# Performance work log

Measured on AMD Instinct MI355X. Metric: run time of the kernel, lower is better.

The kernel has to match this reference:

```python
import jax, jax.numpy as jnp
import numpy as np

DIM = 1024
NUM_HEADS = 16
HEAD_DIM = DIM // NUM_HEADS


def setup_inputs() -> dict:
    key = jax.random.key(0)
    ks = jax.random.split(key, 16)
    B, Sx, Sy = 4, 1024, 1024
    s = 1.0 / np.sqrt(DIM)
    inp = {
        'x': jax.random.normal(ks[0], (B, Sx, DIM), dtype=jnp.float32),
        'y': jax.random.normal(ks[1], (B, Sy, DIM), dtype=jnp.float32),
    }
    names = ['Kx', 'Qx', 'Vx', 'Ky', 'Vy', 'out']
    for i, n in enumerate(names):
        inp[f'W_{n}'] = jax.random.uniform(ks[2 + 2 * i], (DIM, DIM), dtype=jnp.float32, minval=-s, maxval=s)
        inp[f'b_{n}'] = jax.random.uniform(ks[3 + 2 * i], (DIM,), dtype=jnp.float32, minval=-s, maxval=s)
    return inp


def _heads(t, B, S):
    # [B, S, DIM] -> [B, H, S, Dh]
    return t.reshape(B, S, NUM_HEADS, HEAD_DIM).transpose(0, 2, 1, 3)


def _attn(x, y, W_Kx, b_Kx, W_Qx, b_Qx, W_Vx, b_Vx, W_Ky, b_Ky, W_Vy, b_Vy, W_out, b_out):
    B, Sx, _ = x.shape
    Sy = y.shape[1]
    lin = lambda t, W, b: t @ W.T + b
    Q = _heads(lin(x, W_Qx, b_Qx), B, Sx)
    Kc = jnp.concatenate([_heads(lin(x, W_Kx, b_Kx), B, Sx), _heads(lin(y, W_Ky, b_Ky), B, Sy)], axis=2)
    Vc = jnp.concatenate([_heads(lin(x, W_Vx, b_Vx), B, Sx), _heads(lin(y, W_Vy, b_Vy), B, Sy)], axis=2)
    scores = jnp.einsum('bhqd,bhkd->bhqk', Q, Kc) / np.sqrt(HEAD_DIM).astype(np.float32)
    w = jax.nn.softmax(scores, axis=-1)
    o = jnp.einsum('bhqk,bhkd->bhqd', w, Vc)  # [B, H, Sx, Dh]
    o = o.transpose(0, 2, 1, 3).reshape(B, Sx, DIM)
    return lin(o, W_out, b_out)


def reference(x, y, W_Kx, b_Kx, W_Qx, b_Qx, W_Vx, b_Vx, W_Ky, b_Ky, W_Vy, b_Vy, W_out, b_out):
    return _attn(x, y, W_Kx, b_Kx, W_Qx, b_Qx, W_Vx, b_Vx, W_Ky, b_Ky, W_Vy, b_Vy, W_out, b_out)
```

## Files before the change

### kernel.cpp

```cpp
#include <hip/hip_runtime.h>

#define DIMN 1024
#define NH 16
#define DH 64
#define SXX 1024
#define SKV 2048

typedef __bf16 bf16x8 __attribute__((ext_vector_type(8)));
typedef float f32x4 __attribute__((ext_vector_type(4)));
typedef unsigned short us8 __attribute__((ext_vector_type(8)));

__device__ __forceinline__ unsigned short f2bs(float f) {
    return (unsigned short)((__builtin_bit_cast(unsigned int, f) + 0x8000u) >> 16);
}
__device__ __forceinline__ void gl_lds16(const void* g, void* l) {
    __builtin_amdgcn_global_load_lds(
        (const __attribute__((address_space(1))) unsigned int*)g,
        (__attribute__((address_space(3))) unsigned int*)l, 16, 0, 0);
}

struct CvtArgs {
    const float* src[8];
    unsigned short* dst[8];
    int start[8];
};
__global__ __launch_bounds__(256) void cvt_all(CvtArgs a) {
    int b = blockIdx.x;
    int r = 0;
#pragma unroll
    for (int i = 1; i < 8; i++) r += (b >= a.start[i]);
    int off = ((b - a.start[r]) * 256 + (int)threadIdx.x) * 8;
    const float* s = a.src[r] + off;
    float4 f0 = *(const float4*)(s);
    float4 f1 = *(const float4*)(s + 4);
    us8 o;
    o[0] = f2bs(f0.x); o[1] = f2bs(f0.y); o[2] = f2bs(f0.z); o[3] = f2bs(f0.w);
    o[4] = f2bs(f1.x); o[5] = f2bs(f1.y); o[6] = f2bs(f1.z); o[7] = f2bs(f1.w);
    *(us8*)(a.dst[r] + off) = o;
}

template<int KIND>
__global__ void gemm_fused(const unsigned short* __restrict__ A,
                           const unsigned short* __restrict__ W,
                           const float* __restrict__ b0, const float* __restrict__ b1,
                           const float* __restrict__ b2,
                           unsigned short* __restrict__ Qd, unsigned short* __restrict__ Kd,
                           unsigned short* __restrict__ Vd, int roff, float qscale,
                           float* __restrict__ outp) {
    __shared__ __align__(16) unsigned short As[128 * 32];
    __shared__ __align__(16) unsigned short Bs[128 * 32];
    const int K = DIMN;
    int tid = threadIdx.x, wave = tid >> 6, lane = tid & 63;
    int l15 = lane & 15, quad = lane >> 4;
    int wm = wave >> 1, wn = wave & 1;
    int m0 = blockIdx.y * 128, n0 = blockIdx.x * 128;

    int srow = wave * 16 + (lane >> 2);
    int sc8 = (lane & 3) * 8;
    const unsigned short* gA0 = A + (size_t)(m0 + srow) * K + sc8;
    const unsigned short* gA1 = A + (size_t)(m0 + srow + 64) * K + sc8;
    const unsigned short* gW0 = W + (size_t)(n0 + srow) * K + sc8;
    const unsigned short* gW1 = W + (size_t)(n0 + srow + 64) * K + sc8;
    unsigned short* lA0 = As + wave * 512;
    unsigned short* lA1 = As + 2048 + wave * 512;
    unsigned short* lB0 = Bs + wave * 512;
    unsigned short* lB1 = Bs + 2048 + wave * 512;

    f32x4 acc[4][4] = {};
    for (int k0 = 0; k0 < K; k0 += 32) {
        if (k0) __syncthreads();
        gl_lds16(gA0 + k0, lA0);
        gl_lds16(gA1 + k0, lA1);
        gl_lds16(gW0 + k0, lB0);
        gl_lds16(gW1 + k0, lB1);
        __syncthreads();
        bf16x8 af[4], bf[4];
#pragma unroll
        for (int mi = 0; mi < 4; mi++)
            af[mi] = __builtin_bit_cast(bf16x8, *(const us8*)(&As[(wm * 64 + mi * 16 + l15) * 32 + quad * 8]));
#pragma unroll
        for (int ni = 0; ni < 4; ni++)
            bf[ni] = __builtin_bit_cast(bf16x8, *(const us8*)(&Bs[(wn * 64 + ni * 16 + l15) * 32 + quad * 8]));
#pragma unroll
        for (int mi = 0; mi < 4; mi++)
#pragma unroll
            for (int ni = 0; ni < 4; ni++)
                acc[mi][ni] = __builtin_amdgcn_mfma_f32_16x16x32_bf16(af[mi], bf[ni], acc[mi][ni], 0, 0, 0);
    }

    int which = n0 >> 10;
    const float* bp = (which == 0) ? b0 : (which == 1) ? b1 : b2;
    int role;
    if (KIND == 2) role = 3;
    else if (KIND == 1) role = which ? 2 : 0;
    else role = (which == 0) ? 0 : (which == 1) ? 1 : 2;
    float sc = (role == 1) ? qscale : 1.0f;

#pragma unroll
    for (int mi = 0; mi < 4; mi++) {
        int mbase = m0 + wm * 64 + mi * 16 + quad * 4;
#pragma unroll
        for (int ni = 0; ni < 4; ni++) {
            int n = n0 + wn * 64 + ni * 16 + l15;
            int nl = n & 1023;
            float bv = bp[nl];
#pragma unroll
            for (int r = 0; r < 4; r++) {
                float v = (acc[mi][ni][r] + bv) * sc;
                int mm = mbase + r;
                int bidx = mm >> 10, s = mm & 1023, h = nl >> 6, d = nl & 63;
                if (role == 3) {
                    outp[(size_t)mm * DIMN + n] = v;
                } else if (role == 0) {
                    Kd[((size_t)(bidx * NH + h) * SKV + s + roff) * DH + d] = f2bs(v);
                } else if (role == 1) {
                    Qd[((size_t)(bidx * NH + h) * SXX + s) * DH + d] = f2bs(v);
                } else {
                    Vd[((size_t)(bidx * NH + h) * DH + d) * SKV + s + roff] = f2bs(v);
                }
            }
        }
    }
}

__global__ __launch_bounds__(256, 4) void flash_attn(
        const unsigned short* __restrict__ Qb,
        const unsigned short* __restrict__ Kc,
        const unsigned short* __restrict__ Vt,
        unsigned short* __restrict__ Ob) {
    __shared__ __align__(16) unsigned short Ks[2][64 * 64];
    __shared__ __align__(16) unsigned short Vs[2][64 * 64];
    __shared__ __align__(16) unsigned short Ps[4][16 * 64];
    int tid = threadIdx.x, wave = tid >> 6, lane = tid & 63;
    int l15 = lane & 15, quad = lane >> 4;
    int bh = blockIdx.y;
    int qbase = blockIdx.x * 64 + wave * 16;

    const unsigned short* Qp = Qb + ((size_t)bh * SXX + qbase) * DH;
    bf16x8 bq0 = __builtin_bit_cast(bf16x8, *(const us8*)(&Qp[l15 * DH + quad * 8]));
    bf16x8 bq1 = __builtin_bit_cast(bf16x8, *(const us8*)(&Qp[l15 * DH + 32 + quad * 8]));

    const unsigned short* Kg = Kc + (size_t)bh * SKV * DH;
    const unsigned short* Vg = Vt + (size_t)bh * DH * SKV;

    int srow_lo = 8 * wave + (lane >> 3);
    int srow_hi = srow_lo + 32;
    int swz = ((lane & 7) ^ (lane >> 3)) * 8;
    int sl = (lane & 7) * 8;

    us8 pk0, pk1, pv0, pv1;
    auto gload = [&](int c) {
        pk0 = *(const us8*)(Kg + (size_t)(c + srow_lo) * DH + swz);
        pk1 = *(const us8*)(Kg + (size_t)(c + srow_hi) * DH + swz);
        pv0 = *(const us8*)(Vg + (size_t)srow_lo * SKV + c + swz);
        pv1 = *(const us8*)(Vg + (size_t)srow_hi * SKV + c + swz);
    };
    auto lstore = [&](int buf) {
        *(us8*)(&Ks[buf][srow_lo * 64 + sl]) = pk0;
        *(us8*)(&Ks[buf][srow_hi * 64 + sl]) = pk1;
        *(us8*)(&Vs[buf][srow_lo * 64 + sl]) = pv0;
        *(us8*)(&Vs[buf][srow_hi * 64 + sl]) = pv1;
    };

    f32x4 o[4] = {};
    float lsum = 0.0f;

    gload(0);
    lstore(0);
    __syncthreads();

    for (int c = 0; c < SKV; c += 64) {
        int cur = (c >> 6) & 1;
        bool more = (c + 64) < SKV;
        if (more) gload(c + 64);

        const unsigned short* ks = &Ks[cur][0];
        f32x4 st[4];
        int cA = quad ^ (l15 & 7);
#pragma unroll
        for (int ni = 0; ni < 4; ni++) {
            int row = (ni * 16 + l15) * 64;
            bf16x8 ak0 = __builtin_bit_cast(bf16x8, *(const us8*)(ks + row + cA * 8));
            bf16x8 ak1 = __builtin_bit_cast(bf16x8, *(const us8*)(ks + row + (cA ^ 4) * 8));
            f32x4 z = {};
            z = __builtin_amdgcn_mfma_f32_16x16x32_bf16(ak0, bq0, z, 0, 0, 0);
            z = __builtin_amdgcn_mfma_f32_16x16x32_bf16(ak1, bq1, z, 0, 0, 0);
            st[ni] = z;
        }

        unsigned short* pw = &Ps[wave][0];
#pragma unroll
        for (int ni = 0; ni < 4; ni++) {
            float p0 = __builtin_amdgcn_exp2f(st[ni][0]);
            float p1 = __builtin_amdgcn_exp2f(st[ni][1]);
            float p2 = __builtin_amdgcn_exp2f(st[ni][2]);
            float p3 = __builtin_amdgcn_exp2f(st[ni][3]);
            lsum += (p0 + p1) + (p2 + p3);
            unsigned int lo = ((__builtin_bit_cast(unsigned int, p0) + 0x8000u) >> 16)
                            | ((__builtin_bit_cast(unsigned int, p1) + 0x8000u) & 0xffff0000u);
            unsigned int hi = ((__builtin_bit_cast(unsigned int, p2) + 0x8000u) >> 16)
                            | ((__builtin_bit_cast(unsigned int, p3) + 0x8000u) & 0xffff0000u);
            int c8p = (2 * ni + (quad >> 1)) ^ (l15 & 7);
            *(uint2*)(pw + l15 * 64 + c8p * 8 + (quad & 1) * 4) = make_uint2(lo, hi);
        }

        bf16x8 ap0 = __builtin_bit_cast(bf16x8, *(const us8*)(pw + l15 * 64 + cA * 8));
        bf16x8 ap1 = __builtin_bit_cast(bf16x8, *(const us8*)(pw + l15 * 64 + (cA ^ 4) * 8));

        const unsigned short* vs = &Vs[cur][0];
#pragma unroll
        for (int ni = 0; ni < 4; ni++) {
            int row = (ni * 16 + l15) * 64;
            bf16x8 v0 = __builtin_bit_cast(bf16x8, *(const us8*)(vs + row + cA * 8));
            bf16x8 v1 = __builtin_bit_cast(bf16x8, *(const us8*)(vs + row + (cA ^ 4) * 8));
            o[ni] = __builtin_amdgcn_mfma_f32_16x16x32_bf16(ap0, v0, o[ni], 0, 0, 0);
            o[ni] = __builtin_amdgcn_mfma_f32_16x16x32_bf16(ap1, v1, o[ni], 0, 0, 0);
        }

        if (more) lstore(1 - cur);
        __syncthreads();
    }

    lsum += __shfl_xor(lsum, 16);
    lsum += __shfl_xor(lsum, 32);
    int b = bh >> 4, h = bh & 15;
#pragma unroll
    for (int r = 0; r < 4; r++) {
        float lt = __shfl(lsum, quad * 4 + r);
        float inv = __builtin_amdgcn_rcpf(lt);
        int q = qbase + quad * 4 + r;
#pragma unroll
        for (int ni = 0; ni < 4; ni++)
            Ob[((size_t)b * SXX + q) * DIMN + h * DH + ni * 16 + l15] = f2bs(o[ni][r] * inv);
    }
}

extern "C" void kernel_launch(void* const* d_in, const int* in_sizes, int n_in,
                              void* d_out, int out_size, void* d_ws, size_t ws_size,
                              hipStream_t stream) {
    (void)in_sizes; (void)n_in; (void)out_size; (void)ws_size;
    const float* x     = (const float*)d_in[0];
    const float* y     = (const float*)d_in[1];
    const float* W_Kx  = (const float*)d_in[2];
    const float* b_Kx  = (const float*)d_in[3];
    const float* W_Qx  = (const float*)d_in[4];
    const float* b_Qx  = (const float*)d_in[5];
    const float* W_Vx  = (const float*)d_in[6];
    const float* b_Vx  = (const float*)d_in[7];
    const float* W_Ky  = (const float*)d_in[8];
    const float* b_Ky  = (const float*)d_in[9];
    const float* W_Vy  = (const float*)d_in[10];
    const float* b_Vy  = (const float*)d_in[11];
    const float* W_out = (const float*)d_in[12];
    const float* b_out = (const float*)d_in[13];
    float* out = (float*)d_out;

    char* ws = (char*)d_ws;
    unsigned short* xb  = (unsigned short*)(ws);
    unsigned short* yb  = (unsigned short*)(ws + (size_t)( 8 << 20));
    unsigned short* Qb  = (unsigned short*)(ws + (size_t)(16 << 20));
    unsigned short* Kcw = (unsigned short*)(ws + (size_t)(24 << 20));
    unsigned short* Vtw = (unsigned short*)(ws + (size_t)(40 << 20));
    unsigned short* Obw = (unsigned short*)(ws + (size_t)(56 << 20));
    unsigned short* Wb  = (unsigned short*)(ws + (size_t)(64 << 20));

    CvtArgs ca;
    ca.src[0] = x;     ca.dst[0] = xb;                 ca.start[0] = 0;
    ca.src[1] = y;     ca.dst[1] = yb;                 ca.start[1] = 2048;
    ca.src[2] = W_Kx;  ca.dst[2] = Wb + 0u * 1048576;  ca.start[2] = 4096;
    ca.src[3] = W_Qx;  ca.dst[3] = Wb + 1u * 1048576;  ca.start[3] = 4608;
    ca.src[4] = W_Vx;  ca.dst[4] = Wb + 2u * 1048576;  ca.start[4] = 5120;
    ca.src[5] = W_Ky;  ca.dst[5] = Wb + 3u * 1048576;  ca.start[5] = 5632;
    ca.src[6] = W_Vy;  ca.dst[6] = Wb + 4u * 1048576;  ca.start[6] = 6144;
    ca.src[7] = W_out; ca.dst[7] = Wb + 5u * 1048576;  ca.start[7] = 6656;
    cvt_all<<<7168, 256, 0, stream>>>(ca);

    const float qscale = 0.125f * 1.44269504088896340736f;
    gemm_fused<0><<<dim3(24, 32), 256, 0, stream>>>(xb, Wb, b_Kx, b_Qx, b_Vx,
                                                    Qb, Kcw, Vtw, 0, qscale, nullptr);
    gemm_fused<1><<<dim3(16, 32), 256, 0, stream>>>(yb, Wb + 3u * 1048576, b_Ky, b_Vy, nullptr,
                                                    Qb, Kcw, Vtw, 1024, 1.0f, nullptr);
    flash_attn<<<dim3(16, 64), 256, 0, stream>>>(Qb, Kcw, Vtw, Obw);
    gemm_fused<2><<<dim3(8, 32), 256, 0, stream>>>(Obw, Wb + 5u * 1048576, b_out, nullptr, nullptr,
                                                   nullptr, nullptr, nullptr, 0, 1.0f, out);
}
```

Measured before the change: 276.5 us.

## Restructure projection GEMMs and double query tile per wave in attention

```diff
diff --git a/kernel.cpp b/kernel.cpp
--- a/kernel.cpp
+++ b/kernel.cpp
@@ -39,106 +39,176 @@
     *(us8*)(a.dst[r] + off) = o;
 }
 
-template<int KIND>
-__global__ void gemm_fused(const unsigned short* __restrict__ A,
-                           const unsigned short* __restrict__ W,
-                           const float* __restrict__ b0, const float* __restrict__ b1,
-                           const float* __restrict__ b2,
-                           unsigned short* __restrict__ Qd, unsigned short* __restrict__ Kd,
-                           unsigned short* __restrict__ Vd, int roff, float qscale,
-                           float* __restrict__ outp) {
-    __shared__ __align__(16) unsigned short As[128 * 32];
-    __shared__ __align__(16) unsigned short Bs[128 * 32];
+__device__ __forceinline__ void gemm_core(const unsigned short* __restrict__ A,
+                                          const unsigned short* __restrict__ W,
+                                          unsigned short* As, unsigned short* Bs,
+                                          int m0, int n0, f32x4 (&acc)[4][4]) {
     const int K = DIMN;
     int tid = threadIdx.x, wave = tid >> 6, lane = tid & 63;
     int l15 = lane & 15, quad = lane >> 4;
     int wm = wave >> 1, wn = wave & 1;
-    int m0 = blockIdx.y * 128, n0 = blockIdx.x * 128;
-
-    int srow = wave * 16 + (lane >> 2);
-    int sc8 = (lane & 3) * 8;
-    const unsigned short* gA0 = A + (size_t)(m0 + srow) * K + sc8;
-    const unsigned short* gA1 = A + (size_t)(m0 + srow + 64) * K + sc8;
-    const unsigned short* gW0 = W + (size_t)(n0 + srow) * K + sc8;
-    const unsigned short* gW1 = W + (size_t)(n0 + srow + 64) * K + sc8;
-    unsigned short* lA0 = As + wave * 512;
-    unsigned short* lA1 = As + 2048 + wave * 512;
-    unsigned short* lB0 = Bs + wave * 512;
-    unsigned short* lB1 = Bs + 2048 + wave * 512;
+    int srow = wave * 8 + (lane >> 3);
+    int gcol = ((lane & 7) ^ (lane >> 3)) * 8;
+    const unsigned short* gA = A + (size_t)(m0 + srow) * K + gcol;
+    const unsigned short* gW = W + (size_t)(n0 + srow) * K + gcol;
+    unsigned short* lA = As + wave * 512;
+    unsigned short* lB = Bs + wave * 512;
+    int slot0 = (quad ^ (l15 & 7)) * 8;
+
+    for (int k0 = 0; k0 < K; k0 += 64) {
+        if (k0) __syncthreads();
+#pragma unroll
+        for (int j = 0; j < 4; j++) {
+            gl_lds16(gA + k0 + (size_t)j * 32 * K, lA + j * 2048);
+            gl_lds16(gW + k0 + (size_t)j * 32 * K, lB + j * 2048);
+        }
+        __syncthreads();
+#pragma unroll
+        for (int kk = 0; kk < 2; kk++) {
+            int sl = slot0 ^ (kk * 32);
+            bf16x8 af[4], bf[4];
+#pragma unroll
+            for (int mi = 0; mi < 4; mi++)
+                af[mi] = __builtin_bit_cast(bf16x8, *(const us8*)(&As[(wm * 64 + mi * 16 + l15) * 64 + sl]));
+#pragma unroll
+            for (int ni = 0; ni < 4; ni++)
+                bf[ni] = __builtin_bit_cast(bf16x8, *(const us8*)(&Bs[(wn * 64 + ni * 16 + l15) * 64 + sl]));
+#pragma unroll
+            for (int mi = 0; mi < 4; mi++)
+#pragma unroll
+                for (int ni = 0; ni < 4; ni++)
+                    acc[mi][ni] = __builtin_amdgcn_mfma_f32_16x16x32_bf16(af[mi], bf[ni], acc[mi][ni], 0, 0, 0);
+        }
+    }
+}
+
+__global__ __launch_bounds__(256, 2) void gemm_kq(
+        const unsigned short* __restrict__ xb, const unsigned short* __restrict__ yb,
+        const unsigned short* __restrict__ Wb,
+        const float* __restrict__ b_Kx, const float* __restrict__ b_Qx, const float* __restrict__ b_Ky,
+        unsigned short* __restrict__ Qd, unsigned short* __restrict__ Kd, float qscale) {
+    __shared__ __align__(16) unsigned short As[128 * 64];
+    __shared__ __align__(16) unsigned short Bs[128 * 64];
+    int which = blockIdx.x >> 3;
+    int n0 = (blockIdx.x & 7) * 128, m0 = blockIdx.y * 128;
+    const unsigned short* A = (which == 2) ? yb : xb;
+    const unsigned short* W = Wb + (size_t)((which == 0) ? 0 : (which == 1) ? 1 : 3) * 1048576;
+    const float* bp = (which == 0) ? b_Kx : (which == 1) ? b_Qx : b_Ky;
+    int roff = (which == 2) ? 1024 : 0;
+    float sc = (which == 1) ? qscale : 1.0f;
 
     f32x4 acc[4][4] = {};
-    for (int k0 = 0; k0 < K; k0 += 32) {
-        if (k0) __syncthreads();
-        gl_lds16(gA0 + k0, lA0);
-        gl_lds16(gA1 + k0, lA1);
-        gl_lds16(gW0 + k0, lB0);
-        gl_lds16(gW1 + k0, lB1);
-        __syncthreads();
-        bf16x8 af[4], bf[4];
-#pragma unroll
-        for (int mi = 0; mi < 4; mi++)
-            af[mi] = __builtin_bit_cast(bf16x8, *(const us8*)(&As[(wm * 64 + mi * 16 + l15) * 32 + quad * 8]));
-#pragma unroll
-        for (int ni = 0; ni < 4; ni++)
-            bf[ni] = __builtin_bit_cast(bf16x8, *(const us8*)(&Bs[(wn * 64 + ni * 16 + l15) * 32 + quad * 8]));
-#pragma unroll
-        for (int mi = 0; mi < 4; mi++)
-#pragma unroll
-            for (int ni = 0; ni < 4; ni++)
-                acc[mi][ni] = __builtin_amdgcn_mfma_f32_16x16x32_bf16(af[mi], bf[ni], acc[mi][ni], 0, 0, 0);
-    }
-
-    int which = n0 >> 10;
-    const float* bp = (which == 0) ? b0 : (which == 1) ? b1 : b2;
-    int role;
-    if (KIND == 2) role = 3;
-    else if (KIND == 1) role = which ? 2 : 0;
-    else role = (which == 0) ? 0 : (which == 1) ? 1 : 2;
-    float sc = (role == 1) ? qscale : 1.0f;
-
+    gemm_core(A, W, As, Bs, m0, n0, acc);
+
+    int tid = threadIdx.x, wave = tid >> 6, lane = tid & 63;
+    int l15 = lane & 15, quad = lane >> 4;
+    int wm = wave >> 1, wn = wave & 1;
 #pragma unroll
     for (int mi = 0; mi < 4; mi++) {
         int mbase = m0 + wm * 64 + mi * 16 + quad * 4;
 #pragma unroll
         for (int ni = 0; ni < 4; ni++) {
             int n = n0 + wn * 64 + ni * 16 + l15;
-            int nl = n & 1023;
-            float bv = bp[nl];
+            float bv = bp[n];
+            int h = n >> 6, d = n & 63;
 #pragma unroll
             for (int r = 0; r < 4; r++) {
                 float v = (acc[mi][ni][r] + bv) * sc;
                 int mm = mbase + r;
-                int bidx = mm >> 10, s = mm & 1023, h = nl >> 6, d = nl & 63;
-                if (role == 3) {
-                    outp[(size_t)mm * DIMN + n] = v;
-                } else if (role == 0) {
+                int bidx = mm >> 10, s = mm & 1023;
+                if (which == 1)
+                    Qd[((size_t)(bidx * NH + h) * SXX + s) * DH + d] = f2bs(v);
+                else
                     Kd[((size_t)(bidx * NH + h) * SKV + s + roff) * DH + d] = f2bs(v);
-                } else if (role == 1) {
-                    Qd[((size_t)(bidx * NH + h) * SXX + s) * DH + d] = f2bs(v);
-                } else {
-                    Vd[((size_t)(bidx * NH + h) * DH + d) * SKV + s + roff] = f2bs(v);
-                }
             }
         }
     }
 }
 
-__global__ __launch_bounds__(256, 4) void flash_attn(
+__global__ __launch_bounds__(256, 2) void gemm_v(
+        const unsigned short* __restrict__ xb, const unsigned short* __restrict__ yb,
+        const unsigned short* __restrict__ Wb,
+        const float* __restrict__ b_Vx, const float* __restrict__ b_Vy,
+        unsigned short* __restrict__ Vd) {
+    __shared__ __align__(16) unsigned short As[128 * 64];
+    __shared__ __align__(16) unsigned short Bs[128 * 64];
+    int side = blockIdx.y >> 3;
+    int m0 = (blockIdx.y & 7) * 128, n0 = blockIdx.x * 128;
+    const unsigned short* Wv = Wb + (size_t)(side ? 4 : 2) * 1048576;
+    const unsigned short* act = side ? yb : xb;
+    const float* bp = side ? b_Vy : b_Vx;
+    int roff = side ? 1024 : 0;
+
+    f32x4 acc[4][4] = {};
+    gemm_core(Wv, act, As, Bs, m0, n0, acc);
+
+    int tid = threadIdx.x, wave = tid >> 6, lane = tid & 63;
+    int l15 = lane & 15, quad = lane >> 4;
+    int wm = wave >> 1, wn = wave & 1;
+#pragma unroll
+    for (int mi = 0; mi < 4; mi++) {
+        int mbase = m0 + wm * 64 + mi * 16 + quad * 4;
+#pragma unroll
+        for (int ni = 0; ni < 4; ni++) {
+            int n = n0 + wn * 64 + ni * 16 + l15;
+            int bidx = n >> 10, s = n & 1023;
+#pragma unroll
+            for (int r = 0; r < 4; r++) {
+                int m = mbase + r;
+                int h = m >> 6, d = m & 63;
+                float v = acc[mi][ni][r] + bp[m];
+                Vd[((size_t)(bidx * NH + h) * DH + d) * SKV + s + roff] = f2bs(v);
+            }
+        }
+    }
+}
+
+__global__ __launch_bounds__(256, 2) void gemm_out(
+        const unsigned short* __restrict__ Ob, const unsigned short* __restrict__ Wo,
+        const float* __restrict__ bo, float* __restrict__ outp) {
+    __shared__ __align__(16) unsigned short As[128 * 64];
+    __shared__ __align__(16) unsigned short Bs[128 * 64];
+    int n0 = blockIdx.x * 128, m0 = blockIdx.y * 128;
+    f32x4 acc[4][4] = {};
+    gemm_core(Ob, Wo, As, Bs, m0, n0, acc);
+
+    int tid = threadIdx.x, wave = tid >> 6, lane = tid & 63;
+    int l15 = lane & 15, quad = lane >> 4;
+    int wm = wave >> 1, wn = wave & 1;
+#pragma unroll
+    for (int mi = 0; mi < 4; mi++) {
+        int mbase = m0 + wm * 64 + mi * 16 + quad * 4;
+#pragma unroll
+        for (int ni = 0; ni < 4; ni++) {
+            int n = n0 + wn * 64 + ni * 16 + l15;
+            float bv = bo[n];
+#pragma unroll
+            for (int r = 0; r < 4; r++)
+                outp[(size_t)(mbase + r) * DIMN + n] = acc[mi][ni][r] + bv;
+        }
+    }
+}
+
+__global__ __launch_bounds__(256, 2) void flash_attn(
         const unsigned short* __restrict__ Qb,
         const unsigned short* __restrict__ Kc,
         const unsigned short* __restrict__ Vt,
         unsigned short* __restrict__ Ob) {
     __shared__ __align__(16) unsigned short Ks[2][64 * 64];
     __shared__ __align__(16) unsigned short Vs[2][64 * 64];
-    __shared__ __align__(16) unsigned short Ps[4][16 * 64];
-    int tid = threadIdx.x, wave = tid >> 6, lane = tid & 63;
-    int l15 = lane & 15, quad = lane >> 4;
-    int bh = blockIdx.y;
-    int qbase = blockIdx.x * 64 + wave * 16;
+    __shared__ __align__(16) unsigned short Ps[4][32 * 64];
+    int tid = threadIdx.x, wave = tid >> 6, lane = tid & 63;
+    int l15 = lane & 15, quad = lane >> 4;
+    int bh = blockIdx.x;
+    int qbase = blockIdx.y * 128 + wave * 32;
 
     const unsigned short* Qp = Qb + ((size_t)bh * SXX + qbase) * DH;
-    bf16x8 bq0 = __builtin_bit_cast(bf16x8, *(const us8*)(&Qp[l15 * DH + quad * 8]));
-    bf16x8 bq1 = __builtin_bit_cast(bf16x8, *(const us8*)(&Qp[l15 * DH + 32 + quad * 8]));
+    bf16x8 bq[2][2];
+#pragma unroll
+    for (int qt = 0; qt < 2; qt++) {
+        bq[qt][0] = __builtin_bit_cast(bf16x8, *(const us8*)(&Qp[(qt * 16 + l15) * DH + quad * 8]));
+        bq[qt][1] = __builtin_bit_cast(bf16x8, *(const us8*)(&Qp[(qt * 16 + l15) * DH + 32 + quad * 8]));
+    }
 
     const unsigned short* Kg = Kc + (size_t)bh * SKV * DH;
     const unsigned short* Vg = Vt + (size_t)bh * DH * SKV;
@@ -162,8 +232,9 @@
         *(us8*)(&Vs[buf][srow_hi * 64 + sl]) = pv1;
     };
 
-    f32x4 o[4] = {};
-    float lsum = 0.0f;
+    f32x4 o[2][4] = {};
+    float lsum[2] = {0.f, 0.f};
+    int cA = (quad ^ (l15 & 7)) * 8;
 
     gload(0);
     lstore(0);
@@ -175,63 +246,74 @@
         if (more) gload(c + 64);
 
         const unsigned short* ks = &Ks[cur][0];
-        f32x4 st[4];
-        int cA = quad ^ (l15 & 7);
+        bf16x8 ak0[4], ak1[4];
 #pragma unroll
         for (int ni = 0; ni < 4; ni++) {
             int row = (ni * 16 + l15) * 64;
-            bf16x8 ak0 = __builtin_bit_cast(bf16x8, *(const us8*)(ks + row + cA * 8));
-            bf16x8 ak1 = __builtin_bit_cast(bf16x8, *(const us8*)(ks + row + (cA ^ 4) * 8));
-            f32x4 z = {};
-            z = __builtin_amdgcn_mfma_f32_16x16x32_bf16(ak0, bq0, z, 0, 0, 0);
-            z = __builtin_amdgcn_mfma_f32_16x16x32_bf16(ak1, bq1, z, 0, 0, 0);
-            st[ni] = z;
+            ak0[ni] = __builtin_bit_cast(bf16x8, *(const us8*)(ks + row + cA));
+            ak1[ni] = __builtin_bit_cast(bf16x8, *(const us8*)(ks + row + (cA ^ 32)));
         }
 
         unsigned short* pw = &Ps[wave][0];
 #pragma unroll
-        for (int ni = 0; ni < 4; ni++) {
-            float p0 = __builtin_amdgcn_exp2f(st[ni][0]);
-            float p1 = __builtin_amdgcn_exp2f(st[ni][1]);
-            float p2 = __builtin_amdgcn_exp2f(st[ni][2]);
-            float p3 = __builtin_amdgcn_exp2f(st[ni][3]);
-            lsum += (p0 + p1) + (p2 + p3);
-            unsigned int lo = ((__builtin_bit_cast(unsigned int, p0) + 0x8000u) >> 16)
-                            | ((__builtin_bit_cast(unsigned int, p1) + 0x8000u) & 0xffff0000u);
-            unsigned int hi = ((__builtin_bit_cast(unsigned int, p2) + 0x8000u) >> 16)
-                            | ((__builtin_bit_cast(unsigned int, p3) + 0x8000u) & 0xffff0000u);
-            int c8p = (2 * ni + (quad >> 1)) ^ (l15 & 7);
-            *(uint2*)(pw + l15 * 64 + c8p * 8 + (quad & 1) * 4) = make_uint2(lo, hi);
-        }
-
-        bf16x8 ap0 = __builtin_bit_cast(bf16x8, *(const us8*)(pw + l15 * 64 + cA * 8));
-        bf16x8 ap1 = __builtin_bit_cast(bf16x8, *(const us8*)(pw + l15 * 64 + (cA ^ 4) * 8));
+        for (int qt = 0; qt < 2; qt++) {
+#pragma unroll
+            for (int ni = 0; ni < 4; ni++) {
+                f32x4 z = {};
+                z = __builtin_amdgcn_mfma_f32_16x16x32_bf16(ak0[ni], bq[qt][0], z, 0, 0, 0);
+                z = __builtin_amdgcn_mfma_f32_16x16x32_bf16(ak1[ni], bq[qt][1], z, 0, 0, 0);
+                float p0 = __builtin_amdgcn_exp2f(z[0]);
+                float p1 = __builtin_amdgcn_exp2f(z[1]);
+                float p2 = __builtin_amdgcn_exp2f(z[2]);
+                float p3 = __builtin_amdgcn_exp2f(z[3]);
+                lsum[qt] += (p0 + p1) + (p2 + p3);
+                unsigned int lo = ((__builtin_bit_cast(unsigned int, p0) + 0x8000u) >> 16)
+                                | ((__builtin_bit_cast(unsigned int, p1) + 0x8000u) & 0xffff0000u);
+                unsigned int hi = ((__builtin_bit_cast(unsigned int, p2) + 0x8000u) >> 16)
+                                | ((__builtin_bit_cast(unsigned int, p3) + 0x8000u) & 0xffff0000u);
+                int c8p = (2 * ni + (quad >> 1)) ^ (l15 & 7);
+                *(uint2*)(pw + (qt * 16 + l15) * 64 + c8p * 8 + (quad & 1) * 4) = make_uint2(lo, hi);
+            }
+        }
 
         const unsigned short* vs = &Vs[cur][0];
+        bf16x8 av0[4], av1[4];
 #pragma unroll
         for (int ni = 0; ni < 4; ni++) {
             int row = (ni * 16 + l15) * 64;
-            bf16x8 v0 = __builtin_bit_cast(bf16x8, *(const us8*)(vs + row + cA * 8));
-            bf16x8 v1 = __builtin_bit_cast(bf16x8, *(const us8*)(vs + row + (cA ^ 4) * 8));
-            o[ni] = __builtin_amdgcn_mfma_f32_16x16x32_bf16(ap0, v0, o[ni], 0, 0, 0);
-            o[ni] = __builtin_amdgcn_mfma_f32_16x16x32_bf16(ap1, v1, o[ni], 0, 0, 0);
+            av0[ni] = __builtin_bit_cast(bf16x8, *(const us8*)(vs + row + cA));
+            av1[ni] = __builtin_bit_cast(bf16x8, *(const us8*)(vs + row + (cA ^ 32)));
+        }
+#pragma unroll
+        for (int qt = 0; qt < 2; qt++) {
+            bf16x8 ap0 = __builtin_bit_cast(bf16x8, *(const us8*)(pw + (qt * 16 + l15) * 64 + cA));
+            bf16x8 ap1 = __builtin_bit_cast(bf16x8, *(const us8*)(pw + (qt * 16 + l15) * 64 + (cA ^ 32)));
+#pragma unroll
+            for (int ni = 0; ni < 4; ni++) {
+                o[qt][ni] = __builtin_amdgcn_mfma_f32_16x16x32_bf16(ap0, av0[ni], o[qt][ni], 0, 0, 0);
+                o[qt][ni] = __builtin_amdgcn_mfma_f32_16x16x32_bf16(ap1, av1[ni], o[qt][ni], 0, 0, 0);
+            }
         }
 
         if (more) lstore(1 - cur);
         __syncthreads();
     }
 
-    lsum += __shfl_xor(lsum, 16);
-    lsum += __shfl_xor(lsum, 32);
     int b = bh >> 4, h = bh & 15;
 #pragma unroll
-    for (int r = 0; r < 4; r++) {
-        float lt = __shfl(lsum, quad * 4 + r);
-        float inv = __builtin_amdgcn_rcpf(lt);
-        int q = qbase + quad * 4 + r;
-#pragma unroll
-        for (int ni = 0; ni < 4; ni++)
-            Ob[((size_t)b * SXX + q) * DIMN + h * DH + ni * 16 + l15] = f2bs(o[ni][r] * inv);
+    for (int qt = 0; qt < 2; qt++) {
+        float ls = lsum[qt];
+        ls += __shfl_xor(ls, 16);
+        ls += __shfl_xor(ls, 32);
+#pragma unroll
+        for (int r = 0; r < 4; r++) {
+            float lt = __shfl(ls, quad * 4 + r);
+            float inv = __builtin_amdgcn_rcpf(lt);
+            int q = qbase + qt * 16 + quad * 4 + r;
+#pragma unroll
+            for (int ni = 0; ni < 4; ni++)
+                Ob[((size_t)b * SXX + q) * DIMN + h * DH + ni * 16 + l15] = f2bs(o[qt][ni][r] * inv);
+        }
     }
 }
 
@@ -276,11 +358,8 @@
     cvt_all<<<7168, 256, 0, stream>>>(ca);
 
     const float qscale = 0.125f * 1.44269504088896340736f;
-    gemm_fused<0><<<dim3(24, 32), 256, 0, stream>>>(xb, Wb, b_Kx, b_Qx, b_Vx,
-                                                    Qb, Kcw, Vtw, 0, qscale, nullptr);
-    gemm_fused<1><<<dim3(16, 32), 256, 0, stream>>>(yb, Wb + 3u * 1048576, b_Ky, b_Vy, nullptr,
-                                                    Qb, Kcw, Vtw, 1024, 1.0f, nullptr);
-    flash_attn<<<dim3(16, 64), 256, 0, stream>>>(Qb, Kcw, Vtw, Obw);
-    gemm_fused<2><<<dim3(8, 32), 256, 0, stream>>>(Obw, Wb + 5u * 1048576, b_out, nullptr, nullptr,
-                                                   nullptr, nullptr, nullptr, 0, 1.0f, out);
-}
+    gemm_kq<<<dim3(24, 32), 256, 0, stream>>>(xb, yb, Wb, b_Kx, b_Qx, b_Ky, Qb, Kcw, qscale);
+    gemm_v<<<dim3(32, 16), 256, 0, stream>>>(xb, yb, Wb, b_Vx, b_Vy, Vtw);
+    flash_attn<<<dim3(64, 8), 256, 0, stream>>>(Qb, Kcw, Vtw, Obw);
+    gemm_out<<<dim3(8, 32), 256, 0, stream>>>(Obw, Wb + 5u * 1048576, b_out, out);
+}
```

New measurement: 256.4 us. -7.3%, faster.
